# Kernel optimization log

Measured on AMD Instinct MI355X. Metric: run time of the kernel, lower is better.

## Reference

```python
import jax, jax.numpy as jnp
import numpy as np

NEG = -10000.0
EMB = 64
HID = 128


def _lstm_dir(x_tbf, Wih, Whh, b):
    # x_tbf: [T, B, EMB]; Wih: [4H, EMB]; Whh: [4H, H]; b: [4H]
    B = x_tbf.shape[1]
    h0 = jnp.zeros((B, HID), x_tbf.dtype)
    c0 = jnp.zeros((B, HID), x_tbf.dtype)

    def step(carry, xt):
        h, c = carry
        z = xt @ Wih.T + h @ Whh.T + b  # [B, 4H]
        i, f, g, o = jnp.split(z, 4, axis=-1)
        c = jax.nn.sigmoid(f) * c + jax.nn.sigmoid(i) * jnp.tanh(g)
        h = jax.nn.sigmoid(o) * jnp.tanh(c)
        return (h, c), h

    _, hs = jax.lax.scan(step, (h0, c0), x_tbf)
    return hs  # [T, B, H]


def _crf_logZ(feats, trans):
    # feats: [B, T, K]; trans[next, prev]
    B, T, K = feats.shape
    fv0 = jnp.full((B, K), NEG, feats.dtype).at[:, 0].set(0.0)

    def step(fv, emit_t):  # fv [B,K], emit_t [B,K]
        s = fv[:, None, :] + trans[None, :, :] + emit_t[:, :, None]  # [B,next,prev]
        return jax.nn.logsumexp(s, axis=2), None

    fv, _ = jax.lax.scan(step, fv0, jnp.swapaxes(feats, 0, 1))
    return jax.nn.logsumexp(fv + trans[0][None, :], axis=1)  # [B]


def _gold_score(feats, tags, trans):
    # feats: [B,T,K], tags: [B,T]
    B, T, K = feats.shape
    prev = jnp.concatenate([jnp.zeros((B, 1), tags.dtype), tags[:, :-1]], axis=1)
    trans_sc = trans[tags, prev].sum(axis=1)  # [B]
    emit_sc = jnp.take_along_axis(feats, tags[:, :, None], axis=2)[..., 0].sum(axis=1)
    stop_sc = trans[0, tags[:, -1]]
    return trans_sc + emit_sc + stop_sc


def setup_inputs() -> dict:
    key = jax.random.key(0)
    ks = jax.random.split(key, 12)
    V, K, B, T = 32000, 32, 128, 512
    sentences = jax.random.randint(ks[0], (B, T), 0, V)
    tags = jax.random.randint(ks[1], (B, T), 0, K)
    emb = jax.random.normal(ks[2], (V, EMB), jnp.float32) * 0.1
    s_ih = 1.0 / np.sqrt(HID)
    Wih_f = jax.random.uniform(ks[3], (4 * HID, EMB), jnp.float32, -s_ih, s_ih)
    Whh_f = jax.random.uniform(ks[4], (4 * HID, HID), jnp.float32, -s_ih, s_ih)
    b_f = jax.random.uniform(ks[5], (4 * HID,), jnp.float32, -s_ih, s_ih)
    Wih_b = jax.random.uniform(ks[6], (4 * HID, EMB), jnp.float32, -s_ih, s_ih)
    Whh_b = jax.random.uniform(ks[7], (4 * HID, HID), jnp.float32, -s_ih, s_ih)
    b_b = jax.random.uniform(ks[8], (4 * HID,), jnp.float32, -s_ih, s_ih)
    s_o = 1.0 / np.sqrt(2 * HID)
    W_out = jax.random.uniform(ks[9], (K, 2 * HID), jnp.float32, -s_o, s_o)
    b_out = jax.random.uniform(ks[10], (K,), jnp.float32, -s_o, s_o)
    trans = jax.random.normal(ks[11], (K, K), jnp.float32)
    trans = trans.at[:, 0].set(NEG).at[0, :].set(NEG)
    return {"sentences": sentences, "tags": tags, "emb": emb,
            "Wih_f": Wih_f, "Whh_f": Whh_f, "b_f": b_f,
            "Wih_b": Wih_b, "Whh_b": Whh_b, "b_b": b_b,
            "W_out": W_out, "b_out": b_out, "trans": trans}


def reference(sentences, tags, emb, Wih_f, Whh_f, b_f, Wih_b, Whh_b, b_b, W_out, b_out, trans):
    x = emb[sentences]                      # [B, T, EMB]
    x_tbf = jnp.swapaxes(x, 0, 1)           # [T, B, EMB]
    h_f = _lstm_dir(x_tbf, Wih_f, Whh_f, b_f)
    h_b = _lstm_dir(x_tbf[::-1], Wih_b, Whh_b, b_b)[::-1]
    h = jnp.concatenate([h_f, h_b], axis=-1)  # [T, B, 256]
    feats = jnp.swapaxes(h, 0, 1) @ W_out.T + b_out  # [B, T, K]
    logZ = _crf_logZ(feats, trans)
    gold = _gold_score(feats, tags, trans)
    return logZ.sum() - gold.sum()
```

## Files before the change

kernel.cpp:

```cpp
#include <hip/hip_runtime.h>
#include <stdint.h>

typedef short bf16x8 __attribute__((ext_vector_type(8)));
typedef float f32x4 __attribute__((ext_vector_type(4)));

#define NEG (-10000.0f)
#define LOG2E 1.44269504089f
#define LN2 0.69314718056f
#define EXP2F(x) __builtin_amdgcn_exp2f(x)
#define LOG2F(x) __builtin_amdgcn_logf(x)
#define RCPF(x) __builtin_amdgcn_rcpf(x)
constexpr int T_LEN = 512;
constexpr int BATCH = 128;

__device__ __forceinline__ unsigned short f2bf(float f) {
    union { float f; unsigned u; } v; v.f = f;
    return (unsigned short)((v.u + 0x7FFFu + ((v.u >> 16) & 1u)) >> 16);
}
__device__ __forceinline__ float bf2f(unsigned short s) {
    union { unsigned u; float f; } v; v.u = (unsigned)s << 16; return v.f;
}
__device__ __forceinline__ unsigned short f2bf_fast(float f) {
    unsigned r;
    asm("v_cvt_pk_bf16_f32 %0, %1, %2" : "=v"(r) : "v"(f), "v"(f));
    return (unsigned short)r;
}
__device__ __forceinline__ float rlanef(float x, int l) {
    union { float f; int i; } a, r;
    a.f = x;
    r.i = __builtin_amdgcn_readlane(a.i, l);
    return r.f;
}
__device__ __forceinline__ f32x4 mfma16(bf16x8 a, bf16x8 b, f32x4 c) {
    return __builtin_amdgcn_mfma_f32_16x16x32_bf16(a, b, c, 0, 0, 0);
}

__global__ void __launch_bounds__(256) k_embed(const int* __restrict__ sent,
                                               const float* __restrict__ emb,
                                               unsigned short* __restrict__ xt) {
    int gid = blockIdx.x * 256 + threadIdx.x;
    int row = gid >> 5;
    int p   = gid & 31;
    int w = sent[row];
    float2 v = *(const float2*)(emb + (size_t)w * 64 + p * 2);
    unsigned o;
    asm("v_cvt_pk_bf16_f32 %0, %1, %2" : "=v"(o) : "v"(v.x), "v"(v.y));
    ((unsigned*)xt)[(size_t)row * 32 + p] = o;
}

__global__ void __launch_bounds__(512, 2) k_lstm(
        const unsigned short* __restrict__ xt,
        const float* __restrict__ Wih_f, const float* __restrict__ Whh_f, const float* __restrict__ b_f,
        const float* __restrict__ Wih_b, const float* __restrict__ Whh_b, const float* __restrict__ b_b,
        unsigned short* __restrict__ hbuf) {
    const int tid  = threadIdx.x;
    const int lane = tid & 63;
    const int w    = tid >> 6;
    const int b    = blockIdx.x & 127;
    const int dir  = blockIdx.x >> 7;

    const float* Wih  = dir ? Wih_b : Wih_f;
    const float* Whh  = dir ? Whh_b : Whh_f;
    const float* bias = dir ? b_b   : b_f;

    __shared__ __align__(16) unsigned short zbuf[2][32][512];
    __shared__ __align__(16) unsigned short hl[2][128];

    const int nlo = lane & 15;
    const int kg  = lane >> 4;
    const int u   = 16 * w + nlo;

    bf16x8 hfrag[4][4];
    #pragma unroll
    for (int g = 0; g < 4; ++g) {
        const float sc = (g == 2) ? (-2.0f * LOG2E) : (-LOG2E);
        const int j = 128 * g + u;
        #pragma unroll
        for (int kt = 0; kt < 4; ++kt) {
            const float* src = Whh + (size_t)j * 128 + 32 * kt + kg * 8;
            bf16x8 tmp;
            #pragma unroll
            for (int q = 0; q < 8; ++q) tmp[q] = (short)f2bf(src[q] * sc);
            hfrag[g][kt] = tmp;
        }
    }
    bf16x8 wx[4][2];
    float bsc[4];
    #pragma unroll
    for (int nt = 0; nt < 4; ++nt) {
        const int n = 64 * w + 16 * nt + nlo;
        const float scn = ((n >> 7) == 2) ? (-2.0f * LOG2E) : (-LOG2E);
        bsc[nt] = bias[n] * scn;
        #pragma unroll
        for (int kt = 0; kt < 2; ++kt) {
            const float* src = Wih + (size_t)n * 64 + 32 * kt + kg * 8;
            bf16x8 tmp;
            #pragma unroll
            for (int q = 0; q < 8; ++q) tmp[q] = (short)f2bf(src[q] * scn);
            wx[nt][kt] = tmp;
        }
    }

    const unsigned short* xb = xt + (size_t)b * T_LEN * 64;

    auto load_x = [&](int c, bf16x8 xf[2][2]) {
        const int tb = dir ? (511 - 32 * c) : (32 * c);
        #pragma unroll
        for (int rt = 0; rt < 2; ++rt) {
            const int m = 16 * rt + nlo;
            const int t = dir ? (tb - m) : (tb + m);
            xf[rt][0] = *(const bf16x8*)(xb + t * 64 + kg * 8);
            xf[rt][1] = *(const bf16x8*)(xb + t * 64 + 32 + kg * 8);
        }
    };
    auto zx_phase = [&](int buf, bf16x8 xf[2][2]) {
        #pragma unroll
        for (int rt = 0; rt < 2; ++rt) {
            #pragma unroll
            for (int nt = 0; nt < 4; ++nt) {
                f32x4 a = (f32x4){bsc[nt], bsc[nt], bsc[nt], bsc[nt]};
                a = mfma16(xf[rt][0], wx[nt][0], a);
                a = mfma16(xf[rt][1], wx[nt][1], a);
                const int n = 64 * w + 16 * nt + nlo;
                const int base = (n & 127) * 4 + (n >> 7);
                #pragma unroll
                for (int r = 0; r < 4; ++r)
                    zbuf[buf][16 * rt + 4 * kg + r][base] = f2bf(a[r]);
            }
        }
    };

    if (tid < 128) { hl[0][tid] = 0; hl[1][tid] = 0; }
    bf16x8 xfA[2][2], xfB[2][2];
    load_x(0, xfA);
    zx_phase(0, xfA);
    load_x(1, xfB);
    __syncthreads();

    float c = 0.0f;
    const f32x4 z4 = (f32x4){0.f, 0.f, 0.f, 0.f};
    unsigned short* hbp = hbuf + ((size_t)b * T_LEN + (dir ? 511 : 0)) * 256 + dir * 128 + u;
    const ptrdiff_t hstep = dir ? -256 : 256;

    for (int ch = 0; ch < 16; ++ch) {
        const int p = ch & 1;
        if (ch + 1 < 16) zx_phase(1 - p, p ? xfA : xfB);
        if (ch + 2 < 16) load_x(ch + 2, p ? xfB : xfA);

        #pragma unroll 2
        for (int s = 0; s < 32; ++s) {
            const int hp = (32 * ch + s) & 1;

            const unsigned short* hr = hl[hp];
            bf16x8 h0 = *(const bf16x8*)(hr      + kg * 8);
            bf16x8 h1 = *(const bf16x8*)(hr + 32 + kg * 8);
            bf16x8 h2 = *(const bf16x8*)(hr + 64 + kg * 8);
            bf16x8 h3 = *(const bf16x8*)(hr + 96 + kg * 8);
            ushort4 zv = *(const ushort4*)(&zbuf[p][s][u * 4]);

            f32x4 aiA = mfma16(h0, hfrag[0][0], z4);
            f32x4 afA = mfma16(h0, hfrag[1][0], z4);
            f32x4 agA = mfma16(h0, hfrag[2][0], z4);
            f32x4 aoA = mfma16(h0, hfrag[3][0], z4);
            f32x4 aiB = mfma16(h2, hfrag[0][2], z4);
            f32x4 afB = mfma16(h2, hfrag[1][2], z4);
            f32x4 agB = mfma16(h2, hfrag[2][2], z4);
            f32x4 aoB = mfma16(h2, hfrag[3][2], z4);
            aiA = mfma16(h1, hfrag[0][1], aiA);
            afA = mfma16(h1, hfrag[1][1], afA);
            agA = mfma16(h1, hfrag[2][1], agA);
            aoA = mfma16(h1, hfrag[3][1], aoA);
            aiB = mfma16(h3, hfrag[0][3], aiB);
            afB = mfma16(h3, hfrag[1][3], afB);
            agB = mfma16(h3, hfrag[2][3], agB);
            aoB = mfma16(h3, hfrag[3][3], aoB);

            float zi = (bf2f(zv.x) + aiA[0]) + aiB[0];
            float zf = (bf2f(zv.y) + afA[0]) + afB[0];
            float zg = (bf2f(zv.z) + agA[0]) + agB[0];
            float zo = (bf2f(zv.w) + aoA[0]) + aoB[0];

            float ig = RCPF(1.0f + EXP2F(zi));
            float fg = RCPF(1.0f + EXP2F(zf));
            float tg = 2.0f * RCPF(1.0f + EXP2F(zg)) - 1.0f;
            float og = RCPF(1.0f + EXP2F(zo));
            c = fg * c + ig * tg;
            float tc = 2.0f * RCPF(1.0f + EXP2F(-2.0f * LOG2E * c)) - 1.0f;
            unsigned short hv = f2bf_fast(og * tc);

            if (kg == 0) {
                hl[1 - hp][u] = hv;
                *hbp = hv;
            }
            hbp += hstep;
            __asm__ volatile("" ::: "memory");
            __builtin_amdgcn_s_waitcnt(0xc07f);
            __builtin_amdgcn_s_barrier();
            __asm__ volatile("" ::: "memory");
        }
    }
}

__global__ void __launch_bounds__(256) k_feats(const unsigned short* __restrict__ hbuf,
                                               const float* __restrict__ Wout,
                                               const float* __restrict__ bout,
                                               float* __restrict__ feats) {
    const int lane = threadIdx.x & 63;
    const int wv   = blockIdx.x * 4 + (threadIdx.x >> 6);
    const int nlo  = lane & 15, kg = lane >> 4;

    bf16x8 bw[2][8];
    #pragma unroll
    for (int nt = 0; nt < 2; ++nt) {
        const float* src0 = Wout + (size_t)(nt * 16 + nlo) * 256 + kg * 8;
        #pragma unroll
        for (int kt = 0; kt < 8; ++kt) {
            bf16x8 tmp;
            #pragma unroll
            for (int q = 0; q < 8; ++q) tmp[q] = (short)f2bf(src0[kt * 32 + q]);
            bw[nt][kt] = tmp;
        }
    }
    float bb0 = bout[nlo], bb1 = bout[16 + nlo];

    for (int rg = 0; rg < 4; ++rg) {
        int row0 = wv * 64 + rg * 16;
        f32x4 a0 = {0.f,0.f,0.f,0.f}, a1 = {0.f,0.f,0.f,0.f};
        #pragma unroll
        for (int kt = 0; kt < 8; ++kt) {
            bf16x8 a = *(const bf16x8*)(hbuf + (size_t)(row0 + nlo) * 256 + kt * 32 + kg * 8);
            a0 = mfma16(a, bw[0][kt], a0);
            a1 = mfma16(a, bw[1][kt], a1);
        }
        #pragma unroll
        for (int r = 0; r < 4; ++r) {
            size_t rr = (size_t)(row0 + kg * 4 + r) * 32;
            feats[rr + nlo]      = a0[r] + bb0;
            feats[rr + 16 + nlo] = a1[r] + bb1;
        }
    }
}

__global__ void __launch_bounds__(64) k_crf(const float* __restrict__ feats,
                                            const float* __restrict__ trans,
                                            const int* __restrict__ tags,
                                            float* __restrict__ out) {
    const int b    = blockIdx.x;
    const int lane = threadIdx.x;
    const int k1   = lane & 31;

    __shared__ float str[1024];
    for (int i = lane; i < 1024; i += 64) str[i] = trans[i];

    float E[32];
    float sumE = 0.0f;
    #pragma unroll
    for (int j = 0; j < 32; ++j) {
        E[j] = EXP2F(trans[k1 * 32 + j] * LOG2E);
        sumE += E[j];
    }
    __syncthreads();

    const int* tg = tags + (size_t)b * T_LEN;
    const float* fb = feats + (size_t)b * T_LEN * 32;
    float gsum = 0.0f;
    for (int t = lane; t < T_LEN; t += 64) {
        int cur = tg[t];
        int prev = t ? tg[t - 1] : 0;
        gsum += str[cur * 32 + prev] + fb[(size_t)t * 32 + cur];
    }
    #pragma unroll
    for (int o = 32; o >= 1; o >>= 1) gsum += __shfl_xor(gsum, o);

    float coff = NEG * LOG2E;
    float fv2  = coff + LOG2F(1.0f + sumE) + fb[k1] * LOG2E;
    coff = rlanef(fv2, 16);

    float L[8];
    #pragma unroll
    for (int i = 0; i < 8; ++i) L[i] = fb[(size_t)(1 + i) * 32 + k1];

    for (int t0 = 1; t0 < T_LEN; t0 += 8) {
        float N[8];
        #pragma unroll
        for (int i = 0; i < 8; ++i) {
            const int tn = t0 + 8 + i;
            N[i] = (tn < T_LEN) ? fb[(size_t)tn * 32 + k1] : 0.0f;
        }
        #pragma unroll
        for (int i = 0; i < 8; ++i) {
            if (t0 + i < T_LEN) {
                float u = EXP2F(fv2 - coff);
                float p0 = 0.f, p1 = 0.f, p2 = 0.f, p3 = 0.f;
                #pragma unroll
                for (int j = 0; j < 32; j += 4) {
                    p0 += E[j]     * rlanef(u, j);
                    p1 += E[j + 1] * rlanef(u, j + 1);
                    p2 += E[j + 2] * rlanef(u, j + 2);
                    p3 += E[j + 3] * rlanef(u, j + 3);
                }
                float p = (p0 + p1) + (p2 + p3);
                p = fmaxf(p, 1e-37f);
                fv2  = coff + LOG2F(p) + L[i] * LOG2E;
                coff = rlanef(fv2, 16);
            }
        }
        #pragma unroll
        for (int i = 0; i < 8; ++i) L[i] = N[i];
    }

    float v2 = fv2 + str[k1] * LOG2E;
    float m2 = v2;
    #pragma unroll
    for (int o = 32; o >= 1; o >>= 1) m2 = fmaxf(m2, __shfl_xor(m2, o));
    float e = EXP2F(v2 - m2);
    #pragma unroll
    for (int o = 32; o >= 1; o >>= 1) e += __shfl_xor(e, o);
    float logZ = LN2 * (m2 + LOG2F(e) - 1.0f);

    if (lane == 0) {
        float gold = gsum + str[tg[T_LEN - 1]];
        atomicAdd(out, logZ - gold);
    }
}

extern "C" void kernel_launch(void* const* d_in, const int* in_sizes, int n_in,
                              void* d_out, int out_size, void* d_ws, size_t ws_size,
                              hipStream_t stream) {
    const int*   sent  = (const int*)d_in[0];
    const int*   tags  = (const int*)d_in[1];
    const float* emb   = (const float*)d_in[2];
    const float* Wih_f = (const float*)d_in[3];
    const float* Whh_f = (const float*)d_in[4];
    const float* b_f   = (const float*)d_in[5];
    const float* Wih_b = (const float*)d_in[6];
    const float* Whh_b = (const float*)d_in[7];
    const float* b_b   = (const float*)d_in[8];
    const float* Wout  = (const float*)d_in[9];
    const float* bout  = (const float*)d_in[10];
    const float* trans = (const float*)d_in[11];
    (void)in_sizes; (void)n_in; (void)ws_size;

    char* ws = (char*)d_ws;
    unsigned short* hbuf  = (unsigned short*)ws;
    float*          feats = (float*)(ws + 33554432);
    unsigned short* xt    = (unsigned short*)(ws + 33554432 + 8388608);

    (void)hipMemsetAsync(d_out, 0, sizeof(float) * out_size, stream);
    k_embed<<<8192, 256, 0, stream>>>(sent, emb, xt);
    k_lstm <<<256,  512, 0, stream>>>(xt, Wih_f, Whh_f, b_f, Wih_b, Whh_b, b_b, hbuf);
    k_feats<<<256,  256, 0, stream>>>(hbuf, Wout, bout, feats);
    k_crf  <<<BATCH, 64, 0, stream>>>(feats, trans, tags, (float*)d_out);
}
```

Before: 451.6 us.

## Fuse forward and backward LSTM directions into one block per batch row

Each block now processes both LSTM directions for one sequence, interleaving the two independent recurrences within each timestep so one barrier serves both. The goal is to hide the serial MFMA and transcendental latency of one direction behind the other and to halve the number of barriers per direction. Input-projection weights are no longer cached in registers; they are reloaded and converted per chunk to make room for two sets of recurrent weight fragments. This halves the number of blocks and leaves half the CUs idle, while doubling per-step work in each block.

```diff
diff --git a/kernel.cpp b/kernel.cpp
--- a/kernel.cpp
+++ b/kernel.cpp
@@ -56,143 +56,164 @@
     const int tid  = threadIdx.x;
     const int lane = tid & 63;
     const int w    = tid >> 6;
-    const int b    = blockIdx.x & 127;
-    const int dir  = blockIdx.x >> 7;
-
-    const float* Wih  = dir ? Wih_b : Wih_f;
-    const float* Whh  = dir ? Whh_b : Whh_f;
-    const float* bias = dir ? b_b   : b_f;
-
-    __shared__ __align__(16) unsigned short zbuf[2][32][512];
-    __shared__ __align__(16) unsigned short hl[2][128];
+    const int b    = blockIdx.x;
+
+    __shared__ __align__(16) unsigned short zbuf[2][2][16][512];
+    __shared__ __align__(16) unsigned short hlf[2][128];
+    __shared__ __align__(16) unsigned short hlb[2][128];
 
     const int nlo = lane & 15;
     const int kg  = lane >> 4;
     const int u   = 16 * w + nlo;
 
-    bf16x8 hfrag[4][4];
+    bf16x8 hfF[4][4], hfB[4][4];
     #pragma unroll
     for (int g = 0; g < 4; ++g) {
         const float sc = (g == 2) ? (-2.0f * LOG2E) : (-LOG2E);
         const int j = 128 * g + u;
         #pragma unroll
         for (int kt = 0; kt < 4; ++kt) {
-            const float* src = Whh + (size_t)j * 128 + 32 * kt + kg * 8;
-            bf16x8 tmp;
-            #pragma unroll
-            for (int q = 0; q < 8; ++q) tmp[q] = (short)f2bf(src[q] * sc);
-            hfrag[g][kt] = tmp;
-        }
-    }
-    bf16x8 wx[4][2];
-    float bsc[4];
+            const float* sF = Whh_f + (size_t)j * 128 + 32 * kt + kg * 8;
+            const float* sB = Whh_b + (size_t)j * 128 + 32 * kt + kg * 8;
+            bf16x8 tF, tB;
+            #pragma unroll
+            for (int q = 0; q < 8; ++q) { tF[q] = (short)f2bf(sF[q] * sc); tB[q] = (short)f2bf(sB[q] * sc); }
+            hfF[g][kt] = tF; hfB[g][kt] = tB;
+        }
+    }
+    float bscF[4], bscB[4];
     #pragma unroll
     for (int nt = 0; nt < 4; ++nt) {
         const int n = 64 * w + 16 * nt + nlo;
         const float scn = ((n >> 7) == 2) ? (-2.0f * LOG2E) : (-LOG2E);
-        bsc[nt] = bias[n] * scn;
-        #pragma unroll
-        for (int kt = 0; kt < 2; ++kt) {
-            const float* src = Wih + (size_t)n * 64 + 32 * kt + kg * 8;
-            bf16x8 tmp;
-            #pragma unroll
-            for (int q = 0; q < 8; ++q) tmp[q] = (short)f2bf(src[q] * scn);
-            wx[nt][kt] = tmp;
-        }
+        bscF[nt] = b_f[n] * scn;
+        bscB[nt] = b_b[n] * scn;
     }
 
     const unsigned short* xb = xt + (size_t)b * T_LEN * 64;
 
-    auto load_x = [&](int c, bf16x8 xf[2][2]) {
-        const int tb = dir ? (511 - 32 * c) : (32 * c);
-        #pragma unroll
-        for (int rt = 0; rt < 2; ++rt) {
-            const int m = 16 * rt + nlo;
-            const int t = dir ? (tb - m) : (tb + m);
-            xf[rt][0] = *(const bf16x8*)(xb + t * 64 + kg * 8);
-            xf[rt][1] = *(const bf16x8*)(xb + t * 64 + 32 + kg * 8);
-        }
+    auto load_xF = [&](int c, bf16x8 xf[2]) {
+        const int t = 16 * c + nlo;
+        xf[0] = *(const bf16x8*)(xb + t * 64 + kg * 8);
+        xf[1] = *(const bf16x8*)(xb + t * 64 + 32 + kg * 8);
     };
-    auto zx_phase = [&](int buf, bf16x8 xf[2][2]) {
-        #pragma unroll
-        for (int rt = 0; rt < 2; ++rt) {
-            #pragma unroll
-            for (int nt = 0; nt < 4; ++nt) {
-                f32x4 a = (f32x4){bsc[nt], bsc[nt], bsc[nt], bsc[nt]};
-                a = mfma16(xf[rt][0], wx[nt][0], a);
-                a = mfma16(xf[rt][1], wx[nt][1], a);
-                const int n = 64 * w + 16 * nt + nlo;
-                const int base = (n & 127) * 4 + (n >> 7);
-                #pragma unroll
-                for (int r = 0; r < 4; ++r)
-                    zbuf[buf][16 * rt + 4 * kg + r][base] = f2bf(a[r]);
+    auto load_xB = [&](int c, bf16x8 xf[2]) {
+        const int t = 511 - 16 * c - nlo;
+        xf[0] = *(const bf16x8*)(xb + t * 64 + kg * 8);
+        xf[1] = *(const bf16x8*)(xb + t * 64 + 32 + kg * 8);
+    };
+    auto zx_phase = [&](unsigned short (*zb)[512], const float* Wp, const float* bsc, bf16x8 xf[2]) {
+        #pragma unroll
+        for (int nt = 0; nt < 4; ++nt) {
+            const int n = 64 * w + 16 * nt + nlo;
+            const float scn = ((n >> 7) == 2) ? (-2.0f * LOG2E) : (-LOG2E);
+            const float* src = Wp + (size_t)n * 64 + kg * 8;
+            bf16x8 w0, w1;
+            #pragma unroll
+            for (int q = 0; q < 8; ++q) { w0[q] = (short)f2bf(src[q] * scn); w1[q] = (short)f2bf(src[32 + q] * scn); }
+            f32x4 a = (f32x4){bsc[nt], bsc[nt], bsc[nt], bsc[nt]};
+            a = mfma16(xf[0], w0, a);
+            a = mfma16(xf[1], w1, a);
+            const int base = (n & 127) * 4 + (n >> 7);
+            #pragma unroll
+            for (int r = 0; r < 4; ++r)
+                zb[4 * kg + r][base] = f2bf(a[r]);
+        }
+    };
+
+    if (tid < 128) { hlf[0][tid] = 0; hlf[1][tid] = 0; hlb[0][tid] = 0; hlb[1][tid] = 0; }
+    bf16x8 xF0[2], xF1[2], xB0[2], xB1[2];
+    load_xF(0, xF0); load_xB(0, xB0);
+    zx_phase(zbuf[0][0], Wih_f, bscF, xF0);
+    zx_phase(zbuf[1][0], Wih_b, bscB, xB0);
+    load_xF(1, xF1); load_xB(1, xB1);
+    __syncthreads();
+
+    float cF = 0.0f, cB = 0.0f;
+    const f32x4 z4 = (f32x4){0.f, 0.f, 0.f, 0.f};
+    unsigned short* hbF = hbuf + ((size_t)b * T_LEN) * 256 + u;
+    unsigned short* hbB = hbuf + ((size_t)b * T_LEN + 511) * 256 + 128 + u;
+
+    for (int ch = 0; ch < 32; ++ch) {
+        const int p = ch & 1;
+        if (ch + 1 < 32) {
+            zx_phase(zbuf[0][1 - p], Wih_f, bscF, p ? xF0 : xF1);
+            zx_phase(zbuf[1][1 - p], Wih_b, bscB, p ? xB0 : xB1);
+        }
+        if (ch + 2 < 32) {
+            load_xF(ch + 2, p ? xF1 : xF0);
+            load_xB(ch + 2, p ? xB1 : xB0);
+        }
+
+        for (int s = 0; s < 16; ++s) {
+            const int hp = s & 1;
+
+            ushort4 zvF = *(const ushort4*)(&zbuf[0][p][s][u * 4]);
+            ushort4 zvB = *(const ushort4*)(&zbuf[1][p][s][u * 4]);
+            const unsigned short* hrF = hlf[hp];
+            const unsigned short* hrB = hlb[hp];
+            bf16x8 hF0 = *(const bf16x8*)(hrF      + kg * 8);
+            bf16x8 hF1 = *(const bf16x8*)(hrF + 32 + kg * 8);
+            bf16x8 hF2 = *(const bf16x8*)(hrF + 64 + kg * 8);
+            bf16x8 hF3 = *(const bf16x8*)(hrF + 96 + kg * 8);
+            bf16x8 hB0 = *(const bf16x8*)(hrB      + kg * 8);
+            bf16x8 hB1 = *(const bf16x8*)(hrB + 32 + kg * 8);
+            bf16x8 hB2 = *(const bf16x8*)(hrB + 64 + kg * 8);
+            bf16x8 hB3 = *(const bf16x8*)(hrB + 96 + kg * 8);
+
+            f32x4 aiF = mfma16(hF0, hfF[0][0], z4);
+            f32x4 afF = mfma16(hF0, hfF[1][0], z4);
+            f32x4 agF = mfma16(hF0, hfF[2][0], z4);
+            f32x4 aoF = mfma16(hF0, hfF[3][0], z4);
+            f32x4 aiB = mfma16(hB0, hfB[0][0], z4);
+            f32x4 afB = mfma16(hB0, hfB[1][0], z4);
+            f32x4 agB = mfma16(hB0, hfB[2][0], z4);
+            f32x4 aoB = mfma16(hB0, hfB[3][0], z4);
+            #pragma unroll
+            for (int kt = 1; kt < 4; ++kt) {
+                bf16x8 hhF = (kt == 1) ? hF1 : (kt == 2) ? hF2 : hF3;
+                bf16x8 hhB = (kt == 1) ? hB1 : (kt == 2) ? hB2 : hB3;
+                aiF = mfma16(hhF, hfF[0][kt], aiF);
+                afF = mfma16(hhF, hfF[1][kt], afF);
+                agF = mfma16(hhF, hfF[2][kt], agF);
+                aoF = mfma16(hhF, hfF[3][kt], aoF);
+                aiB = mfma16(hhB, hfB[0][kt], aiB);
+                afB = mfma16(hhB, hfB[1][kt], afB);
+                agB = mfma16(hhB, hfB[2][kt], agB);
+                aoB = mfma16(hhB, hfB[3][kt], aoB);
             }
-        }
-    };
-
-    if (tid < 128) { hl[0][tid] = 0; hl[1][tid] = 0; }
-    bf16x8 xfA[2][2], xfB[2][2];
-    load_x(0, xfA);
-    zx_phase(0, xfA);
-    load_x(1, xfB);
-    __syncthreads();
-
-    float c = 0.0f;
-    const f32x4 z4 = (f32x4){0.f, 0.f, 0.f, 0.f};
-    unsigned short* hbp = hbuf + ((size_t)b * T_LEN + (dir ? 511 : 0)) * 256 + dir * 128 + u;
-    const ptrdiff_t hstep = dir ? -256 : 256;
-
-    for (int ch = 0; ch < 16; ++ch) {
-        const int p = ch & 1;
-        if (ch + 1 < 16) zx_phase(1 - p, p ? xfA : xfB);
-        if (ch + 2 < 16) load_x(ch + 2, p ? xfB : xfA);
-
-        #pragma unroll 2
-        for (int s = 0; s < 32; ++s) {
-            const int hp = (32 * ch + s) & 1;
-
-            const unsigned short* hr = hl[hp];
-            bf16x8 h0 = *(const bf16x8*)(hr      + kg * 8);
-            bf16x8 h1 = *(const bf16x8*)(hr + 32 + kg * 8);
-            bf16x8 h2 = *(const bf16x8*)(hr + 64 + kg * 8);
-            bf16x8 h3 = *(const bf16x8*)(hr + 96 + kg * 8);
-            ushort4 zv = *(const ushort4*)(&zbuf[p][s][u * 4]);
-
-            f32x4 aiA = mfma16(h0, hfrag[0][0], z4);
-            f32x4 afA = mfma16(h0, hfrag[1][0], z4);
-            f32x4 agA = mfma16(h0, hfrag[2][0], z4);
-            f32x4 aoA = mfma16(h0, hfrag[3][0], z4);
-            f32x4 aiB = mfma16(h2, hfrag[0][2], z4);
-            f32x4 afB = mfma16(h2, hfrag[1][2], z4);
-            f32x4 agB = mfma16(h2, hfrag[2][2], z4);
-            f32x4 aoB = mfma16(h2, hfrag[3][2], z4);
-            aiA = mfma16(h1, hfrag[0][1], aiA);
-            afA = mfma16(h1, hfrag[1][1], afA);
-            agA = mfma16(h1, hfrag[2][1], agA);
-            aoA = mfma16(h1, hfrag[3][1], aoA);
-            aiB = mfma16(h3, hfrag[0][3], aiB);
-            afB = mfma16(h3, hfrag[1][3], afB);
-            agB = mfma16(h3, hfrag[2][3], agB);
-            aoB = mfma16(h3, hfrag[3][3], aoB);
-
-            float zi = (bf2f(zv.x) + aiA[0]) + aiB[0];
-            float zf = (bf2f(zv.y) + afA[0]) + afB[0];
-            float zg = (bf2f(zv.z) + agA[0]) + agB[0];
-            float zo = (bf2f(zv.w) + aoA[0]) + aoB[0];
-
-            float ig = RCPF(1.0f + EXP2F(zi));
-            float fg = RCPF(1.0f + EXP2F(zf));
-            float tg = 2.0f * RCPF(1.0f + EXP2F(zg)) - 1.0f;
-            float og = RCPF(1.0f + EXP2F(zo));
-            c = fg * c + ig * tg;
-            float tc = 2.0f * RCPF(1.0f + EXP2F(-2.0f * LOG2E * c)) - 1.0f;
-            unsigned short hv = f2bf_fast(og * tc);
-
-            if (kg == 0) {
-                hl[1 - hp][u] = hv;
-                *hbp = hv;
+
+            {
+                float zi = bf2f(zvF.x), zf = bf2f(zvF.y), zg = bf2f(zvF.z), zo = bf2f(zvF.w);
+                float ig = RCPF(1.0f + EXP2F(aiF[0] + zi));
+                float fg = RCPF(1.0f + EXP2F(afF[0] + zf));
+                float tg = 2.0f * RCPF(1.0f + EXP2F(agF[0] + zg)) - 1.0f;
+                float og = RCPF(1.0f + EXP2F(aoF[0] + zo));
+                cF = fg * cF + ig * tg;
+                float tc = 2.0f * RCPF(1.0f + EXP2F(-2.0f * LOG2E * cF)) - 1.0f;
+                unsigned short hv = f2bf_fast(og * tc);
+                if (kg == 0) {
+                    hlf[1 - hp][u] = hv;
+                    *hbF = hv;
+                }
             }
-            hbp += hstep;
+            hbF += 256;
+            {
+                float zi = bf2f(zvB.x), zf = bf2f(zvB.y), zg = bf2f(zvB.z), zo = bf2f(zvB.w);
+                float ig = RCPF(1.0f + EXP2F(aiB[0] + zi));
+                float fg = RCPF(1.0f + EXP2F(afB[0] + zf));
+                float tg = 2.0f * RCPF(1.0f + EXP2F(agB[0] + zg)) - 1.0f;
+                float og = RCPF(1.0f + EXP2F(aoB[0] + zo));
+                cB = fg * cB + ig * tg;
+                float tc = 2.0f * RCPF(1.0f + EXP2F(-2.0f * LOG2E * cB)) - 1.0f;
+                unsigned short hv = f2bf_fast(og * tc);
+                if (kg == 0) {
+                    hlb[1 - hp][u] = hv;
+                    *hbB = hv;
+                }
+            }
+            hbB -= 256;
+
             __asm__ volatile("" ::: "memory");
             __builtin_amdgcn_s_waitcnt(0xc07f);
             __builtin_amdgcn_s_barrier();
@@ -348,7 +369,7 @@
 
     (void)hipMemsetAsync(d_out, 0, sizeof(float) * out_size, stream);
     k_embed<<<8192, 256, 0, stream>>>(sent, emb, xt);
-    k_lstm <<<256,  512, 0, stream>>>(xt, Wih_f, Whh_f, b_f, Wih_b, Whh_b, b_b, hbuf);
+    k_lstm <<<BATCH, 512, 0, stream>>>(xt, Wih_f, Whh_f, b_f, Wih_b, Whh_b, b_b, hbuf);
     k_feats<<<256,  256, 0, stream>>>(hbuf, Wout, bout, feats);
     k_crf  <<<BATCH, 64, 0, stream>>>(feats, trans, tags, (float*)d_out);
 }
```

New measurement: 949.7 us. +110.3%, slower.
